# Kernel tuning notes

Measured on AMD Instinct MI355X. Metric: run time of the kernel, lower is better.

The kernel has to match this reference:

```python
import jax, jax.numpy as jnp
import numpy as np

N = 100_000   # atoms
B = 10_000    # building blocks
E = 320_000   # edges (bb <- atom)
D = 256       # embed_dim
H = 8         # heads
HD = D // H   # head_dim = 32
DIST = 64     # gaussian dist embed dim
MAX_R = 10.0


def setup_inputs() -> dict:
    key = jax.random.key(0)
    ks = jax.random.split(key, 10)
    atom_feats = jax.random.normal(ks[0], (N, D), jnp.float32)
    coords = jax.random.normal(ks[1], (N, 3), jnp.float32) * 3.0
    bb_vec = jnp.sort(jax.random.randint(ks[2], (N,), 0, B, jnp.int32))
    src = jax.random.randint(ks[3], (E,), 0, N, jnp.int32)
    tgt = jax.random.randint(ks[4], (E,), 0, B, jnp.int32)
    # linear params, [in, out] layout (x @ W + b)
    Wq = jax.random.normal(ks[5], (D, D), jnp.float32) / np.sqrt(D)
    Wk = jax.random.normal(ks[6], (D + DIST, D), jnp.float32) / np.sqrt(D + DIST)
    Wv = jax.random.normal(ks[7], (D + DIST, D), jnp.float32) / np.sqrt(D + DIST)
    Wo = jax.random.normal(ks[8], (D, D), jnp.float32) / np.sqrt(D)
    bq = jnp.zeros((D,), jnp.float32)
    bk = jnp.zeros((D,), jnp.float32)
    bv = jnp.zeros((D,), jnp.float32)
    bo = jnp.zeros((D,), jnp.float32)
    return dict(atom_feats=atom_feats, coords=coords, Wq=Wq, bq=bq, Wk=Wk, bk=bk,
                Wv=Wv, bv=bv, Wo=Wo, bo=bo, bb_vec=bb_vec, src=src, tgt=tgt)


def _gaussian_smearing(dist):
    offsets = jnp.linspace(0.0, MAX_R, DIST)            # [DIST]
    coeff = -0.5 / (offsets[1] - offsets[0]) ** 2
    return jnp.exp(coeff * (dist[:, None] - offsets) ** 2)  # [E, DIST]


def reference(atom_feats, coords, Wq, bq, Wk, bk, Wv, bv, Wo, bo, bb_vec, src, tgt):
    # building-block centers: mean coords, summed feats per bb
    counts = jax.ops.segment_sum(jnp.ones((N,), coords.dtype), bb_vec, num_segments=B)
    bb_center_pos = jax.ops.segment_sum(coords, bb_vec, num_segments=B)
    bb_center_pos = bb_center_pos / jnp.maximum(counts, 1.0)[:, None]       # [B, 3]
    bb_center_feats = jax.ops.segment_sum(atom_feats, bb_vec, num_segments=B)  # [B, D]

    # per-edge distance embedding
    edge_vec = coords[src] - bb_center_pos[tgt]                             # [E, 3]
    dist = jnp.sqrt(jnp.sum(edge_vec * edge_vec, axis=-1))                  # [E]
    edge_dist_embed = _gaussian_smearing(dist)                              # [E, DIST]

    # QKV
    q = (bb_center_feats @ Wq + bq).reshape(B, H, HD)                       # [B, H, HD]
    atom_input = jnp.concatenate([atom_feats[src], edge_dist_embed], -1)    # [E, D+DIST]
    k = (atom_input @ Wk + bk).reshape(E, H, HD)
    v = (atom_input @ Wv + bv).reshape(E, H, HD)

    # per-edge attention logits + segment softmax over tgt
    attn = jnp.einsum('ehc,ehc->eh', q[tgt], k) / np.sqrt(HD)               # [E, H]
    seg_max = jax.ops.segment_max(attn, tgt, num_segments=B)                # [B, H]
    ex = jnp.exp(attn - seg_max[tgt])
    denom = jax.ops.segment_sum(ex, tgt, num_segments=B)                    # [B, H]
    attn = ex / (denom[tgt] + 1e-16)

    # weighted scatter-sum of messages
    msg = attn[..., None] * v                                               # [E, H, HD]
    out = jax.ops.segment_sum(msg, tgt, num_segments=B).reshape(B, D)       # [B, D]
    return out @ Wo + bo
```

## Files before the change

### kernel.cpp

```cpp
#include <hip/hip_runtime.h>
#include <math.h>

#define N_ATOMS 100000
#define B_BB    10000
#define E_EDGES 320000
#define D_DIM   256
#define NHEAD   8
#define NDIST   64
#define EPAD    128

#define DELTA   (10.0f/63.0f)
#define GCOEFF  (-0.5f/(DELTA*DELTA))
#define QKSCALE 0.17677669529663687f

__global__ void k_offsets(const int* __restrict__ bb_vec, int* __restrict__ atom_off,
                          int* __restrict__ edge_cnt) {
  int b = blockIdx.x * 256 + threadIdx.x;
  if (b <= B_BB) {
    int lo = 0, hi = N_ATOMS;
    while (lo < hi) { int mid = (lo + hi) >> 1; if (bb_vec[mid] < b) lo = mid + 1; else hi = mid; }
    atom_off[b] = lo;
  }
  if (b < B_BB) edge_cnt[b] = 0;
}

__global__ __launch_bounds__(256) void k_bb_centers(
    const float* __restrict__ af, const float* __restrict__ coords,
    const int* __restrict__ atom_off, float* __restrict__ bbF, float* __restrict__ bb_pos) {
  int t = threadIdx.x;
  for (int b = blockIdx.x; b < B_BB; b += gridDim.x) {
    int s = atom_off[b], e = atom_off[b + 1];
    float acc = 0.f;
    for (int a = s; a < e; a++) acc += af[(size_t)a * D_DIM + t];
    bbF[(size_t)b * D_DIM + t] = acc;
    if (t < 3) {
      float c = 0.f;
      for (int a = s; a < e; a++) c += coords[(size_t)a * 3 + t];
      float cnt = (float)(e - s);
      bb_pos[b * 4 + t] = c / fmaxf(cnt, 1.0f);
    }
  }
}

__global__ __launch_bounds__(256) void k_gemm256(
    const float* __restrict__ A, const float* __restrict__ W,
    const float* __restrict__ bias, float* __restrict__ C, int M) {
  __shared__ __align__(16) float As[2][16][68];
  __shared__ __align__(16) float Ws[2][16][64];
  int tid = threadIdx.x;
  int tx = tid & 15, ty = tid >> 4;
  int row0 = blockIdx.x * 64, col0 = blockIdx.y * 64;
  int ar = tid >> 2, ac = (tid & 3) * 4;
  int wr = tid >> 4, wc = (tid & 15) * 4;
  int arow = row0 + ar;
  const float* Ap = A + (size_t)arow * 256 + ac;
  const float* Wp = W + (size_t)wr * 256 + col0 + wc;
  float acc[4][4] = {};
  {
    float4 va = make_float4(0.f, 0.f, 0.f, 0.f);
    if (arow < M) va = *(const float4*)Ap;
    As[0][ac + 0][ar] = va.x; As[0][ac + 1][ar] = va.y;
    As[0][ac + 2][ar] = va.z; As[0][ac + 3][ar] = va.w;
    *(float4*)&Ws[0][wr][wc] = *(const float4*)Wp;
  }
  __syncthreads();
  int cur = 0;
  for (int k0 = 0; k0 < 256; k0 += 16) {
    float4 va, vw;
    bool nxt = (k0 + 16) < 256;
    if (nxt) {
      va = make_float4(0.f, 0.f, 0.f, 0.f);
      if (arow < M) va = *(const float4*)(Ap + k0 + 16);
      vw = *(const float4*)(Wp + (size_t)(k0 + 16) * 256);
    }
#pragma unroll
    for (int kk = 0; kk < 16; kk++) {
      float4 a = *(const float4*)&As[cur][kk][ty * 4];
      float4 b = *(const float4*)&Ws[cur][kk][tx * 4];
      float av[4] = {a.x, a.y, a.z, a.w};
      float bv4[4] = {b.x, b.y, b.z, b.w};
#pragma unroll
      for (int i = 0; i < 4; i++)
#pragma unroll
        for (int j = 0; j < 4; j++) acc[i][j] += av[i] * bv4[j];
    }
    if (nxt) {
      As[cur ^ 1][ac + 0][ar] = va.x; As[cur ^ 1][ac + 1][ar] = va.y;
      As[cur ^ 1][ac + 2][ar] = va.z; As[cur ^ 1][ac + 3][ar] = va.w;
      *(float4*)&Ws[cur ^ 1][wr][wc] = vw;
      __syncthreads();
      cur ^= 1;
    }
  }
#pragma unroll
  for (int i = 0; i < 4; i++) {
    int row = row0 + ty * 4 + i;
    if (row < M) {
      int col = col0 + tx * 4;
      float4 r = make_float4(acc[i][0] + bias[col + 0], acc[i][1] + bias[col + 1],
                             acc[i][2] + bias[col + 2], acc[i][3] + bias[col + 3]);
      *(float4*)&C[(size_t)row * 256 + col] = r;
    }
  }
}

__global__ void k_hist(const int* __restrict__ tgt, int* __restrict__ edge_cnt) {
  int e = blockIdx.x * 256 + threadIdx.x;
  if (e < E_EDGES) atomicAdd(&edge_cnt[tgt[e]], 1);
}

__global__ __launch_bounds__(1024) void k_scan(
    const int* __restrict__ edge_cnt, int* __restrict__ edge_start, int* __restrict__ cursor,
    int* __restrict__ src_sorted, float* __restrict__ dist_sorted) {
  __shared__ int ssum[1024];
  int tid = threadIdx.x;
  int base = tid * 10;
  int v[10]; int s = 0;
#pragma unroll
  for (int k = 0; k < 10; k++) { int i = base + k; v[k] = (i < B_BB) ? edge_cnt[i] : 0; s += v[k]; }
  ssum[tid] = s;
  __syncthreads();
  for (int off = 1; off < 1024; off <<= 1) {
    int t = (tid >= off) ? ssum[tid - off] : 0;
    __syncthreads();
    ssum[tid] += t;
    __syncthreads();
  }
  int excl = ssum[tid] - s;
#pragma unroll
  for (int k = 0; k < 10; k++) {
    int i = base + k;
    if (i < B_BB) { edge_start[i] = excl; cursor[i] = excl; }
    excl += v[k];
  }
  if (tid == 1023) edge_start[B_BB] = E_EDGES;
  if (tid < EPAD) { src_sorted[E_EDGES + tid] = 0; dist_sorted[E_EDGES + tid] = 0.f; }
}

__global__ void k_fill(const int* __restrict__ src, const int* __restrict__ tgt,
                       const float* __restrict__ coords, const float* __restrict__ bb_pos,
                       int* __restrict__ cursor, int* __restrict__ src_sorted,
                       float* __restrict__ dist_sorted) {
  int e = blockIdx.x * 256 + threadIdx.x;
  if (e >= E_EDGES) return;
  int b = tgt[e], a = src[e];
  int pos = atomicAdd(&cursor[b], 1);
  float dx = coords[a * 3 + 0] - bb_pos[b * 4 + 0];
  float dy = coords[a * 3 + 1] - bb_pos[b * 4 + 1];
  float dz = coords[a * 3 + 2] - bb_pos[b * 4 + 2];
  src_sorted[pos] = a;
  dist_sorted[pos] = sqrtf(dx * dx + dy * dy + dz * dz);
}

__global__ __launch_bounds__(256) void k_wt(
    const float* __restrict__ q, const float* __restrict__ Wk, float* __restrict__ wt) {
  __shared__ __align__(16) float As[32][132];
  __shared__ __align__(16) float Bs[32][68];
  int tid = threadIdx.x;
  int b0 = blockIdx.x * 128;
  int i0 = blockIdx.y * 64;
  int h  = blockIdx.z;
  {
    int r = tid >> 1, c0 = (tid & 1) * 16;
    int row = b0 + r;
    const float* qp = q + (size_t)row * 256 + h * 32 + c0;
#pragma unroll
    for (int jj = 0; jj < 4; ++jj) {
      float4 v = make_float4(0.f, 0.f, 0.f, 0.f);
      if (row < B_BB) v = *(const float4*)(qp + 4 * jj);
      As[c0 + 4*jj + 0][r] = v.x; As[c0 + 4*jj + 1][r] = v.y;
      As[c0 + 4*jj + 2][r] = v.z; As[c0 + 4*jj + 3][r] = v.w;
    }
  }
  {
    int r = tid >> 2, c0 = (tid & 3) * 8;
    const float* wp = Wk + (size_t)(i0 + r) * 256 + h * 32 + c0;
#pragma unroll
    for (int jj = 0; jj < 2; ++jj) {
      float4 v = *(const float4*)(wp + 4 * jj);
      Bs[c0 + 4*jj + 0][r] = v.x; Bs[c0 + 4*jj + 1][r] = v.y;
      Bs[c0 + 4*jj + 2][r] = v.z; Bs[c0 + 4*jj + 3][r] = v.w;
    }
  }
  __syncthreads();
  int tx = tid & 15, ty = tid >> 4;
  float acc[8][4] = {};
#pragma unroll
  for (int kk = 0; kk < 32; ++kk) {
    float4 a0 = *(const float4*)&As[kk][ty * 8];
    float4 a1 = *(const float4*)&As[kk][ty * 8 + 4];
    float4 b4 = *(const float4*)&Bs[kk][tx * 4];
    float av[8] = {a0.x, a0.y, a0.z, a0.w, a1.x, a1.y, a1.z, a1.w};
    float bv4[4] = {b4.x, b4.y, b4.z, b4.w};
#pragma unroll
    for (int i = 0; i < 8; ++i)
#pragma unroll
      for (int j = 0; j < 4; ++j) acc[i][j] += av[i] * bv4[j];
  }
#pragma unroll
  for (int i = 0; i < 8; ++i) {
    int row = b0 + ty * 8 + i;
    if (row < B_BB) {
      float4 o = make_float4(acc[i][0] * QKSCALE, acc[i][1] * QKSCALE,
                             acc[i][2] * QKSCALE, acc[i][3] * QKSCALE);
      *(float4*)&wt[(size_t)row * 2560 + h * 320 + i0 + tx * 4] = o;
    }
  }
}

#define FMA4(p, v, Wb, k) \
  p = fmaf((v).x, Wb[(k)], p);   p = fmaf((v).y, Wb[(k)+1], p); \
  p = fmaf((v).z, Wb[(k)+2], p); p = fmaf((v).w, Wb[(k)+3], p);

#define ACC4(Sarr, k, ww, v) \
  Sarr[(k)]   = fmaf(ww, (v).x, Sarr[(k)]);   Sarr[(k)+1] = fmaf(ww, (v).y, Sarr[(k)+1]); \
  Sarr[(k)+2] = fmaf(ww, (v).z, Sarr[(k)+2]); Sarr[(k)+3] = fmaf(ww, (v).w, Sarr[(k)+3]);

__global__ __launch_bounds__(256) void k_attn(
    const float* __restrict__ af, float* __restrict__ wtS,
    const int* __restrict__ edge_start, const int* __restrict__ src_sorted,
    const float* __restrict__ dist_sorted, float* __restrict__ wsum) {
  int tid = threadIdx.x;
  int lane = tid & 63;
  int wv = tid >> 6;
  int h0 = 2 * wv, h1 = 2 * wv + 1;
  int g = lane >> 4;
  int sub = lane & 15;
  int b = blockIdx.x;

  int s0 = edge_start[b], e1 = edge_start[b + 1];
  float* wtb = wtS + (size_t)b * 2560;
  const float* wr0 = wtb + h0 * 320;
  const float* wr1 = wtb + h1 * 320;

  float W0[16], W1[16], wd0[4], wd1[4];
#pragma unroll
  for (int j = 0; j < 4; ++j) {
    float4 t0 = *(const float4*)(wr0 + sub * 16 + 4 * j);
    float4 t1 = *(const float4*)(wr1 + sub * 16 + 4 * j);
    W0[4*j+0] = t0.x; W0[4*j+1] = t0.y; W0[4*j+2] = t0.z; W0[4*j+3] = t0.w;
    W1[4*j+0] = t1.x; W1[4*j+1] = t1.y; W1[4*j+2] = t1.z; W1[4*j+3] = t1.w;
  }
#pragma unroll
  for (int j = 0; j < 4; ++j) { wd0[j] = wr0[256 + sub + 16*j]; wd1[j] = wr1[256 + sub + 16*j]; }

  float cj[4];
#pragma unroll
  for (int j = 0; j < 4; ++j) cj[j] = (float)(sub + 16 * j) * DELTA;

  float l0 = 0.f, l1 = 0.f;
  float S0r[16] = {}, S1r[16] = {};
  float sd0[4] = {}, sd1[4] = {};

  if (s0 < e1) {
    int iaC = src_sorted[s0 + 8 + g];
    int iaD = src_sorted[s0 + 12 + g];
    float ddA = dist_sorted[s0 + g];
    float ddB = dist_sorted[s0 + 4 + g];
    float ddC = dist_sorted[s0 + 8 + g];
    float ddD = dist_sorted[s0 + 12 + g];
    int iaA = src_sorted[s0 + g];
    int iaB = src_sorted[s0 + 4 + g];
    const float4* rA = (const float4*)(af + (size_t)iaA * 256 + sub * 16);
    const float4* rB = (const float4*)(af + (size_t)iaB * 256 + sub * 16);
    float4 A0 = rA[0], A1 = rA[1], A2 = rA[2], A3 = rA[3];
    float4 B0 = rB[0], B1 = rB[1], B2 = rB[2], B3 = rB[3];

    for (int eb = s0; eb < e1; eb += 8) {
      int iaC2 = src_sorted[eb + 16 + g];
      float ddC2 = dist_sorted[eb + 16 + g];
      int iaD2 = src_sorted[eb + 20 + g];
      float ddD2 = dist_sorted[eb + 20 + g];
      const float4* rC = (const float4*)(af + (size_t)iaC * 256 + sub * 16);
      float4 C0 = rC[0], C1 = rC[1], C2 = rC[2], C3 = rC[3];

      float embA[4], embB[4];
#pragma unroll
      for (int j = 0; j < 4; ++j) {
        float da = ddA - cj[j]; embA[j] = __expf(GCOEFF * da * da);
        float db = ddB - cj[j]; embB[j] = __expf(GCOEFF * db * db);
      }
      float pA0 = 0.f, pA1 = 0.f, pB0 = 0.f, pB1 = 0.f;
      FMA4(pA0, A0, W0, 0);  FMA4(pA1, A0, W1, 0);
      FMA4(pB0, B0, W0, 0);  FMA4(pB1, B0, W1, 0);
      FMA4(pA0, A1, W0, 4);  FMA4(pA1, A1, W1, 4);
      FMA4(pB0, B1, W0, 4);  FMA4(pB1, B1, W1, 4);
      FMA4(pA0, A2, W0, 8);  FMA4(pA1, A2, W1, 8);
      FMA4(pB0, B2, W0, 8);  FMA4(pB1, B2, W1, 8);
      FMA4(pA0, A3, W0, 12); FMA4(pA1, A3, W1, 12);
      FMA4(pB0, B3, W0, 12); FMA4(pB1, B3, W1, 12);
#pragma unroll
      for (int j = 0; j < 4; ++j) {
        pA0 = fmaf(embA[j], wd0[j], pA0); pA1 = fmaf(embA[j], wd1[j], pA1);
        pB0 = fmaf(embB[j], wd0[j], pB0); pB1 = fmaf(embB[j], wd1[j], pB1);
      }
#pragma unroll
      for (int off = 8; off > 0; off >>= 1) {
        pA0 += __shfl_xor(pA0, off);
        pA1 += __shfl_xor(pA1, off);
        pB0 += __shfl_xor(pB0, off);
        pB1 += __shfl_xor(pB1, off);
      }
      float wA0 = __expf(pA0), wA1 = __expf(pA1);
      float wB0 = __expf(pB0), wB1 = __expf(pB1);
      if (eb + g >= e1)     { wA0 = 0.f; wA1 = 0.f; }
      if (eb + 4 + g >= e1) { wB0 = 0.f; wB1 = 0.f; }
      l0 += wA0 + wB0; l1 += wA1 + wB1;
#pragma unroll
      for (int j = 0; j < 4; ++j) {
        sd0[j] = fmaf(wA0, embA[j], sd0[j]); sd1[j] = fmaf(wA1, embA[j], sd1[j]);
        sd0[j] = fmaf(wB0, embB[j], sd0[j]); sd1[j] = fmaf(wB1, embB[j], sd1[j]);
      }

      ACC4(S0r, 0,  wA0, A0); ACC4(S1r, 0,  wA1, A0);
      ACC4(S0r, 4,  wA0, A1); ACC4(S1r, 4,  wA1, A1);
      ACC4(S0r, 8,  wA0, A2); ACC4(S1r, 8,  wA1, A2);
      ACC4(S0r, 12, wA0, A3); ACC4(S1r, 12, wA1, A3);

      const float4* rD = (const float4*)(af + (size_t)iaD * 256 + sub * 16);
      float4 D0 = rD[0], D1 = rD[1], D2 = rD[2], D3 = rD[3];

      ACC4(S0r, 0,  wB0, B0); ACC4(S1r, 0,  wB1, B0);
      ACC4(S0r, 4,  wB0, B1); ACC4(S1r, 4,  wB1, B1);
      ACC4(S0r, 8,  wB0, B2); ACC4(S1r, 8,  wB1, B2);
      ACC4(S0r, 12, wB0, B3); ACC4(S1r, 12, wB1, B3);

      A0 = C0; A1 = C1; A2 = C2; A3 = C3;
      B0 = D0; B1 = D1; B2 = D2; B3 = D3;
      ddA = ddC; ddB = ddD; ddC = ddC2; ddD = ddD2;
      iaC = iaC2; iaD = iaD2;
    }
  }

#pragma unroll
  for (int off = 16; off <= 32; off <<= 1) {
    l0 += __shfl_xor(l0, off);
    l1 += __shfl_xor(l1, off);
#pragma unroll
    for (int c = 0; c < 16; ++c) {
      S0r[c] += __shfl_xor(S0r[c], off);
      S1r[c] += __shfl_xor(S1r[c], off);
    }
#pragma unroll
    for (int j = 0; j < 4; ++j) {
      sd0[j] += __shfl_xor(sd0[j], off);
      sd1[j] += __shfl_xor(sd1[j], off);
    }
  }

  float inv0 = 1.0f / (l0 + 1e-16f), inv1 = 1.0f / (l1 + 1e-16f);
  if (g == 0) {
#pragma unroll
    for (int j = 0; j < 4; ++j) {
      float4 o0 = make_float4(S0r[4*j+0]*inv0, S0r[4*j+1]*inv0, S0r[4*j+2]*inv0, S0r[4*j+3]*inv0);
      float4 o1 = make_float4(S1r[4*j+0]*inv1, S1r[4*j+1]*inv1, S1r[4*j+2]*inv1, S1r[4*j+3]*inv1);
      *(float4*)(wtb + h0 * 320 + sub * 16 + 4 * j) = o0;
      *(float4*)(wtb + h1 * 320 + sub * 16 + 4 * j) = o1;
    }
#pragma unroll
    for (int j = 0; j < 4; ++j) {
      wtb[h0 * 320 + 256 + sub + 16 * j] = sd0[j] * inv0;
      wtb[h1 * 320 + 256 + sub + 16 * j] = sd1[j] * inv1;
    }
    if (sub == 0) {
      wsum[b * 8 + h0] = l0 * inv0;
      wsum[b * 8 + h1] = l1 * inv1;
    }
  }
}

__global__ __launch_bounds__(256) void k_out_head(
    const float* __restrict__ Sf, const float* __restrict__ Wv,
    const float* __restrict__ bv, const float* __restrict__ wsum,
    float* __restrict__ out_pre) {
  __shared__ __align__(16) float As[32][264];
  __shared__ __align__(16) float Bs[32][36];
  int tid = threadIdx.x;
  int b0 = blockIdx.x * 256;
  int h  = blockIdx.y;
  int tx = tid & 7, ty = tid >> 3;
  float acc[8][4] = {};
  for (int k0 = 0; k0 < 320; k0 += 32) {
    {
      int row = b0 + tid;
      const float* sp = Sf + (size_t)row * 2560 + h * 320 + k0;
#pragma unroll
      for (int jj = 0; jj < 8; ++jj) {
        float4 v = make_float4(0.f, 0.f, 0.f, 0.f);
        if (row < B_BB) v = *(const float4*)(sp + 4 * jj);
        As[4*jj + 0][tid] = v.x; As[4*jj + 1][tid] = v.y;
        As[4*jj + 2][tid] = v.z; As[4*jj + 3][tid] = v.w;
      }
    }
    {
      int r = tid >> 3, c0 = (tid & 7) * 4;
      float4 v = *(const float4*)&Wv[(size_t)(k0 + r) * 256 + h * 32 + c0];
      *(float4*)&Bs[r][c0] = v;
    }
    __syncthreads();
#pragma unroll
    for (int kk = 0; kk < 32; ++kk) {
      float4 a0 = *(const float4*)&As[kk][ty * 8];
      float4 a1 = *(const float4*)&As[kk][ty * 8 + 4];
      float4 b4 = *(const float4*)&Bs[kk][tx * 4];
      float av[8] = {a0.x, a0.y, a0.z, a0.w, a1.x, a1.y, a1.z, a1.w};
      float bv4[4] = {b4.x, b4.y, b4.z, b4.w};
#pragma unroll
      for (int i = 0; i < 8; ++i)
#pragma unroll
        for (int j = 0; j < 4; ++j) acc[i][j] += av[i] * bv4[j];
    }
    __syncthreads();
  }
  float bvv[4];
#pragma unroll
  for (int j = 0; j < 4; ++j) bvv[j] = bv[h * 32 + tx * 4 + j];
#pragma unroll
  for (int i = 0; i < 8; ++i) {
    int row = b0 + ty * 8 + i;
    if (row < B_BB) {
      float ws = wsum[row * 8 + h];
      float4 o = make_float4(acc[i][0] + ws * bvv[0], acc[i][1] + ws * bvv[1],
                             acc[i][2] + ws * bvv[2], acc[i][3] + ws * bvv[3]);
      *(float4*)&out_pre[(size_t)row * 256 + h * 32 + tx * 4] = o;
    }
  }
}

extern "C" void kernel_launch(void* const* d_in, const int* in_sizes, int n_in,
                              void* d_out, int out_size, void* d_ws, size_t ws_size,
                              hipStream_t stream) {
  const float* af     = (const float*)d_in[0];
  const float* coords = (const float*)d_in[1];
  const float* Wq     = (const float*)d_in[2];
  const float* bq     = (const float*)d_in[3];
  const float* Wk     = (const float*)d_in[4];
  const float* bk     = (const float*)d_in[5];  (void)bk;
  const float* Wv     = (const float*)d_in[6];
  const float* bv     = (const float*)d_in[7];
  const float* Wo     = (const float*)d_in[8];
  const float* bo     = (const float*)d_in[9];
  const int* bb_vec   = (const int*)d_in[10];
  const int* src      = (const int*)d_in[11];
  const int* tgt      = (const int*)d_in[12];
  float* out = (float*)d_out;
  (void)in_sizes; (void)n_in; (void)out_size; (void)ws_size;

  char* ws = (char*)d_ws;
  size_t o = 0;
  auto alloc = [&](size_t bytes) { size_t r = o; o += (bytes + 255) & ~(size_t)255; return r; };
  int*   atom_off    = (int*)(ws + alloc((B_BB + 1) * 4));
  int*   edge_cnt    = (int*)(ws + alloc((size_t)B_BB * 4));
  int*   edge_start  = (int*)(ws + alloc((B_BB + 1) * 4));
  int*   cursor      = (int*)(ws + alloc((size_t)B_BB * 4));
  int*   src_sorted  = (int*)(ws + alloc((size_t)(E_EDGES + EPAD) * 4));
  float* dist_sorted = (float*)(ws + alloc((size_t)(E_EDGES + EPAD) * 4));
  float* bbF         = (float*)(ws + alloc((size_t)B_BB * 256 * 4));
  float* bb_pos      = (float*)(ws + alloc((size_t)B_BB * 4 * 4));
  float* q           = (float*)(ws + alloc((size_t)B_BB * 256 * 4));
  float* wtS         = (float*)(ws + alloc((size_t)B_BB * 2560 * 4));
  float* wsum        = (float*)(ws + alloc((size_t)B_BB * 8 * 4));
  float* out_pre     = (float*)(ws + alloc((size_t)B_BB * 256 * 4));

  k_offsets<<<(B_BB + 1 + 255) / 256, 256, 0, stream>>>(bb_vec, atom_off, edge_cnt);
  k_bb_centers<<<2560, 256, 0, stream>>>(af, coords, atom_off, bbF, bb_pos);
  k_hist<<<(E_EDGES + 255) / 256, 256, 0, stream>>>(tgt, edge_cnt);
  k_scan<<<1, 1024, 0, stream>>>(edge_cnt, edge_start, cursor, src_sorted, dist_sorted);
  k_fill<<<(E_EDGES + 255) / 256, 256, 0, stream>>>(src, tgt, coords, bb_pos, cursor,
                                                    src_sorted, dist_sorted);
  k_gemm256<<<dim3((B_BB + 63) / 64, 4), 256, 0, stream>>>(bbF, Wq, bq, q, B_BB);
  k_wt<<<dim3((B_BB + 127) / 128, 5, 8), 256, 0, stream>>>(q, Wk, wtS);
  k_attn<<<B_BB, 256, 0, stream>>>(af, wtS, edge_start, src_sorted, dist_sorted, wsum);
  k_out_head<<<dim3((B_BB + 255) / 256, 8), 256, 0, stream>>>(wtS, Wv, bv, wsum, out_pre);
  k_gemm256<<<dim3((B_BB + 63) / 64, 4), 256, 0, stream>>>(out_pre, Wo, bo, out, B_BB);
}
```

Measured before the change: 569.2 us.

## Fuse per-head Wv projection into attention kernel via LDS, drop out_head kernel

The attention kernel now keeps the normalized weighted sums S (feature and distance parts) and per-head weight sums in shared memory. After the softmax reduction it computes the per-head Wv projection itself, using a 4-way split over the 320-long reduction and a final LDS reduce that adds the bias term. This removes the global write and reread of the 10000x2560 S buffer and one kernel launch. In exchange every block streams the full 320x256 Wv from cache, about 320KB per block across 10000 blocks, and adds LDS use that may lower occupancy.

```diff
diff --git a/kernel.cpp b/kernel.cpp
--- a/kernel.cpp
+++ b/kernel.cpp
@@ -8,6 +8,7 @@
 #define NHEAD   8
 #define NDIST   64
 #define EPAD    128
+#define SLD     324
 
 #define DELTA   (10.0f/63.0f)
 #define GCOEFF  (-0.5f/(DELTA*DELTA))
@@ -217,9 +218,13 @@
   Sarr[(k)+2] = fmaf(ww, (v).z, Sarr[(k)+2]); Sarr[(k)+3] = fmaf(ww, (v).w, Sarr[(k)+3]);
 
 __global__ __launch_bounds__(256) void k_attn(
-    const float* __restrict__ af, float* __restrict__ wtS,
+    const float* __restrict__ af, const float* __restrict__ wtS,
     const int* __restrict__ edge_start, const int* __restrict__ src_sorted,
-    const float* __restrict__ dist_sorted, float* __restrict__ wsum) {
+    const float* __restrict__ dist_sorted, const float* __restrict__ Wv,
+    const float* __restrict__ bv, float* __restrict__ out_pre) {
+  __shared__ __align__(16) float S_lds[NHEAD * SLD];
+  __shared__ float wsum_lds[NHEAD];
+  __shared__ __align__(16) float4 part_lds[4][64];
   int tid = threadIdx.x;
   int lane = tid & 63;
   int wv = tid >> 6;
@@ -229,7 +234,7 @@
   int b = blockIdx.x;
 
   int s0 = edge_start[b], e1 = edge_start[b + 1];
-  float* wtb = wtS + (size_t)b * 2560;
+  const float* wtb = wtS + (size_t)b * 2560;
   const float* wr0 = wtb + h0 * 320;
   const float* wr1 = wtb + h1 * 320;
 
@@ -352,78 +357,64 @@
   if (g == 0) {
 #pragma unroll
     for (int j = 0; j < 4; ++j) {
-      float4 o0 = make_float4(S0r[4*j+0]*inv0, S0r[4*j+1]*inv0, S0r[4*j+2]*inv0, S0r[4*j+3]*inv0);
-      float4 o1 = make_float4(S1r[4*j+0]*inv1, S1r[4*j+1]*inv1, S1r[4*j+2]*inv1, S1r[4*j+3]*inv1);
-      *(float4*)(wtb + h0 * 320 + sub * 16 + 4 * j) = o0;
-      *(float4*)(wtb + h1 * 320 + sub * 16 + 4 * j) = o1;
+      S_lds[h0*SLD + sub*16 + 4*j + 0] = S0r[4*j+0]*inv0;
+      S_lds[h0*SLD + sub*16 + 4*j + 1] = S0r[4*j+1]*inv0;
+      S_lds[h0*SLD + sub*16 + 4*j + 2] = S0r[4*j+2]*inv0;
+      S_lds[h0*SLD + sub*16 + 4*j + 3] = S0r[4*j+3]*inv0;
+      S_lds[h1*SLD + sub*16 + 4*j + 0] = S1r[4*j+0]*inv1;
+      S_lds[h1*SLD + sub*16 + 4*j + 1] = S1r[4*j+1]*inv1;
+      S_lds[h1*SLD + sub*16 + 4*j + 2] = S1r[4*j+2]*inv1;
+      S_lds[h1*SLD + sub*16 + 4*j + 3] = S1r[4*j+3]*inv1;
     }
 #pragma unroll
     for (int j = 0; j < 4; ++j) {
-      wtb[h0 * 320 + 256 + sub + 16 * j] = sd0[j] * inv0;
-      wtb[h1 * 320 + 256 + sub + 16 * j] = sd1[j] * inv1;
+      S_lds[h0*SLD + 256 + sub + 16*j] = sd0[j]*inv0;
+      S_lds[h1*SLD + 256 + sub + 16*j] = sd1[j]*inv1;
     }
     if (sub == 0) {
-      wsum[b * 8 + h0] = l0 * inv0;
-      wsum[b * 8 + h1] = l1 * inv1;
-    }
-  }
-}
-
-__global__ __launch_bounds__(256) void k_out_head(
-    const float* __restrict__ Sf, const float* __restrict__ Wv,
-    const float* __restrict__ bv, const float* __restrict__ wsum,
-    float* __restrict__ out_pre) {
-  __shared__ __align__(16) float As[32][264];
-  __shared__ __align__(16) float Bs[32][36];
-  int tid = threadIdx.x;
-  int b0 = blockIdx.x * 256;
-  int h  = blockIdx.y;
-  int tx = tid & 7, ty = tid >> 3;
-  float acc[8][4] = {};
-  for (int k0 = 0; k0 < 320; k0 += 32) {
-    {
-      int row = b0 + tid;
-      const float* sp = Sf + (size_t)row * 2560 + h * 320 + k0;
-#pragma unroll
-      for (int jj = 0; jj < 8; ++jj) {
-        float4 v = make_float4(0.f, 0.f, 0.f, 0.f);
-        if (row < B_BB) v = *(const float4*)(sp + 4 * jj);
-        As[4*jj + 0][tid] = v.x; As[4*jj + 1][tid] = v.y;
-        As[4*jj + 2][tid] = v.z; As[4*jj + 3][tid] = v.w;
-      }
-    }
-    {
-      int r = tid >> 3, c0 = (tid & 7) * 4;
-      float4 v = *(const float4*)&Wv[(size_t)(k0 + r) * 256 + h * 32 + c0];
-      *(float4*)&Bs[r][c0] = v;
-    }
-    __syncthreads();
-#pragma unroll
-    for (int kk = 0; kk < 32; ++kk) {
-      float4 a0 = *(const float4*)&As[kk][ty * 8];
-      float4 a1 = *(const float4*)&As[kk][ty * 8 + 4];
-      float4 b4 = *(const float4*)&Bs[kk][tx * 4];
-      float av[8] = {a0.x, a0.y, a0.z, a0.w, a1.x, a1.y, a1.z, a1.w};
-      float bv4[4] = {b4.x, b4.y, b4.z, b4.w};
-#pragma unroll
-      for (int i = 0; i < 8; ++i)
-#pragma unroll
-        for (int j = 0; j < 4; ++j) acc[i][j] += av[i] * bv4[j];
-    }
-    __syncthreads();
-  }
-  float bvv[4];
-#pragma unroll
-  for (int j = 0; j < 4; ++j) bvv[j] = bv[h * 32 + tx * 4 + j];
-#pragma unroll
-  for (int i = 0; i < 8; ++i) {
-    int row = b0 + ty * 8 + i;
-    if (row < B_BB) {
-      float ws = wsum[row * 8 + h];
-      float4 o = make_float4(acc[i][0] + ws * bvv[0], acc[i][1] + ws * bvv[1],
-                             acc[i][2] + ws * bvv[2], acc[i][3] + ws * bvv[3]);
-      *(float4*)&out_pre[(size_t)row * 256 + h * 32 + tx * 4] = o;
-    }
+      wsum_lds[h0] = l0 * inv0;
+      wsum_lds[h1] = l1 * inv1;
+    }
+  }
+  __syncthreads();
+
+  {
+    int iq = tid >> 6;
+    int o4 = tid & 63;
+    int hh = o4 >> 3;
+    int c0 = hh * 32 + (o4 & 7) * 4;
+    const float* Sh = S_lds + hh * SLD;
+    const float* Wvp = Wv + c0;
+    float4 a0v = make_float4(0.f, 0.f, 0.f, 0.f);
+    float4 a1v = make_float4(0.f, 0.f, 0.f, 0.f);
+#pragma unroll 8
+    for (int ii = 0; ii < 80; ii += 2) {
+      int i1 = iq + 4*ii, i2 = iq + 4*ii + 4;
+      float s1 = Sh[i1], s2 = Sh[i2];
+      float4 w1 = *(const float4*)(Wvp + (size_t)i1 * 256);
+      float4 w2 = *(const float4*)(Wvp + (size_t)i2 * 256);
+      a0v.x = fmaf(s1, w1.x, a0v.x); a0v.y = fmaf(s1, w1.y, a0v.y);
+      a0v.z = fmaf(s1, w1.z, a0v.z); a0v.w = fmaf(s1, w1.w, a0v.w);
+      a1v.x = fmaf(s2, w2.x, a1v.x); a1v.y = fmaf(s2, w2.y, a1v.y);
+      a1v.z = fmaf(s2, w2.z, a1v.z); a1v.w = fmaf(s2, w2.w, a1v.w);
+    }
+    a0v.x += a1v.x; a0v.y += a1v.y; a0v.z += a1v.z; a0v.w += a1v.w;
+    part_lds[iq][o4] = a0v;
+  }
+  __syncthreads();
+  if (tid < 64) {
+    float4 p0 = part_lds[0][tid], p1 = part_lds[1][tid];
+    float4 p2 = part_lds[2][tid], p3 = part_lds[3][tid];
+    int hh = tid >> 3;
+    int col = hh * 32 + (tid & 7) * 4;
+    float ws = wsum_lds[hh];
+    float4 bvv = *(const float4*)&bv[col];
+    float4 r;
+    r.x = (p0.x + p1.x) + (p2.x + p3.x) + ws * bvv.x;
+    r.y = (p0.y + p1.y) + (p2.y + p3.y) + ws * bvv.y;
+    r.z = (p0.z + p1.z) + (p2.z + p3.z) + ws * bvv.z;
+    r.w = (p0.w + p1.w) + (p2.w + p3.w) + ws * bvv.w;
+    *(float4*)&out_pre[(size_t)b * 256 + col] = r;
   }
 }
 
@@ -458,8 +449,7 @@
   float* bbF         = (float*)(ws + alloc((size_t)B_BB * 256 * 4));
   float* bb_pos      = (float*)(ws + alloc((size_t)B_BB * 4 * 4));
   float* q           = (float*)(ws + alloc((size_t)B_BB * 256 * 4));
-  float* wtS         = (float*)(ws + alloc((size_t)B_BB * 2560 * 4));
-  float* wsum        = (float*)(ws + alloc((size_t)B_BB * 8 * 4));
+  float* wt          = (float*)(ws + alloc((size_t)B_BB * 2560 * 4));
   float* out_pre     = (float*)(ws + alloc((size_t)B_BB * 256 * 4));
 
   k_offsets<<<(B_BB + 1 + 255) / 256, 256, 0, stream>>>(bb_vec, atom_off, edge_cnt);
@@ -469,8 +459,8 @@
   k_fill<<<(E_EDGES + 255) / 256, 256, 0, stream>>>(src, tgt, coords, bb_pos, cursor,
                                                     src_sorted, dist_sorted);
   k_gemm256<<<dim3((B_BB + 63) / 64, 4), 256, 0, stream>>>(bbF, Wq, bq, q, B_BB);
-  k_wt<<<dim3((B_BB + 127) / 128, 5, 8), 256, 0, stream>>>(q, Wk, wtS);
-  k_attn<<<B_BB, 256, 0, stream>>>(af, wtS, edge_start, src_sorted, dist_sorted, wsum);
-  k_out_head<<<dim3((B_BB + 255) / 256, 8), 256, 0, stream>>>(wtS, Wv, bv, wsum, out_pre);
+  k_wt<<<dim3((B_BB + 127) / 128, 5, 8), 256, 0, stream>>>(q, Wk, wt);
+  k_attn<<<B_BB, 256, 0, stream>>>(af, wt, edge_start, src_sorted, dist_sorted,
+                                   Wv, bv, out_pre);
   k_gemm256<<<dim3((B_BB + 63) / 64, 4), 256, 0, stream>>>(out_pre, Wo, bo, out, B_BB);
 }
```

Result: slower. 605.8 us (+6.4%).
